# Kernel optimization log

Hardware: AMD Instinct MI355X
Metric: run time of the kernel (lower is better)

## Reference

```python
import jax, jax.numpy as jnp
import numpy as np

N_NODES = 50000
N_EDGES = 600000
D_IN = 128
D = 128
N_REL = 2
N_LAYERS = 3


def rgcn_conv(h, src, dst, edge_type, weight, root, bias):
    # PyG RGCNConv (no bases), aggr='mean' per relation:
    # out_i = h_i @ root + bias + sum_r mean_{j in N_r(i)} h_j @ W_r
    out = h @ root + bias                      # [N, D]
    hs = h[src]                                # [E, D] gather once
    for r in range(N_REL):
        mask = (edge_type == r).astype(h.dtype)          # [E]
        agg = jax.ops.segment_sum(hs * mask[:, None], dst, num_segments=N_NODES)  # [N, D]
        cnt = jax.ops.segment_sum(mask, dst, num_segments=N_NODES)                # [N]
        mean = agg / jnp.maximum(cnt, 1.0)[:, None]
        out = out + mean @ weight[r]
    return out


def setup_inputs() -> dict:
    key = jax.random.key(0)
    ks = jax.random.split(key, 10)
    x = jax.random.normal(ks[0], (N_NODES, D_IN), dtype=jnp.float32)
    edge_index = jax.random.randint(ks[1], (2, N_EDGES), 0, N_NODES, dtype=jnp.int64)
    edge_attr = jax.random.normal(ks[2], (N_EDGES, N_REL), dtype=jnp.float32)
    # input projection f: Linear(D_IN, D); stored as [D_IN, D] (apply as x @ Wf + bf)
    Wf = jax.random.normal(ks[3], (D_IN, D), dtype=jnp.float32) / np.sqrt(D_IN)
    bf = jnp.zeros((D,), dtype=jnp.float32)
    # per-layer RGCNConv params, stacked over layers
    conv_weight = jax.random.normal(ks[4], (N_LAYERS, N_REL, D, D), dtype=jnp.float32) / np.sqrt(D)
    conv_root = jax.random.normal(ks[5], (N_LAYERS, D, D), dtype=jnp.float32) / np.sqrt(D)
    conv_bias = jnp.zeros((N_LAYERS, D), dtype=jnp.float32)
    return {"x": x, "edge_index": edge_index, "edge_attr": edge_attr,
            "Wf": Wf, "bf": bf, "conv_weight": conv_weight,
            "conv_root": conv_root, "conv_bias": conv_bias}


def reference(x, edge_index, edge_attr, Wf, bf, conv_weight, conv_root, conv_bias):
    src, dst = edge_index[0], edge_index[1]
    edge_type = jnp.argmax(edge_attr, axis=1)           # [E]
    h = jax.nn.relu(x @ Wf + bf)                        # [N, D]
    for l in range(N_LAYERS):
        h = rgcn_conv(h, src, dst, edge_type, conv_weight[l], conv_root[l], conv_bias[l])
        h = jax.nn.relu(h)
    return h
```

## Files before the change

### kernel.cpp

```cpp
#include <hip/hip_runtime.h>
#include <hip/hip_bf16.h>

#define NN 50000
#define NE 600000
#define D 128
#define NREL 2
#define BM 128

typedef __attribute__((ext_vector_type(8))) short bf16x8;
typedef __attribute__((ext_vector_type(4))) float f32x4;

__device__ __forceinline__ float bf2f(short s) {
    return __uint_as_float(((unsigned int)(unsigned short)s) << 16);
}

__global__ void k_etype_count(const float* __restrict__ attr,
                              const int* __restrict__ dst,
                              int* __restrict__ etype,
                              int* __restrict__ cnt, int E) {
    int i = blockIdx.x * blockDim.x + threadIdx.x;
    if (i >= E) return;
    float2 a = reinterpret_cast<const float2*>(attr)[i];
    int r = (a.y > a.x) ? 1 : 0;
    etype[i] = r;
    atomicAdd(&cnt[r * NN + dst[i]], 1);
}

__global__ void k_inv(const int* __restrict__ cnt, float* __restrict__ inv) {
    int i = blockIdx.x * blockDim.x + threadIdx.x;
    if (i >= NREL * NN) return;
    int c = cnt[i];
    inv[i] = 1.0f / (float)(c > 1 ? c : 1);
}

__global__ void k_alloc(const int* __restrict__ cnt, int* __restrict__ off,
                        int* __restrict__ total) {
    int i = blockIdx.x * blockDim.x + threadIdx.x;
    if (i >= NREL * NN) return;
    off[i] = atomicAdd(total, cnt[i]);
}

__global__ void k_fill(const int* __restrict__ src, const int* __restrict__ dst,
                       const int* __restrict__ etype,
                       int* __restrict__ cursor, int* __restrict__ srcs, int E) {
    int i = blockIdx.x * blockDim.x + threadIdx.x;
    if (i >= E) return;
    int key = etype[i] * NN + dst[i];
    int pos = atomicAdd(&cursor[key], 1);
    srcs[pos] = src[i];
}

__global__ void k_cvt_x(const float* __restrict__ x,
                        __hip_bfloat16* __restrict__ xb, int n4) {
    int i = blockIdx.x * blockDim.x + threadIdx.x;
    if (i >= n4) return;
    float4 v = reinterpret_cast<const float4*>(x)[i];
    __hip_bfloat162 a = __float22bfloat162_rn(make_float2(v.x, v.y));
    __hip_bfloat162 b = __float22bfloat162_rn(make_float2(v.z, v.w));
    reinterpret_cast<__hip_bfloat162*>(xb)[i * 2 + 0] = a;
    reinterpret_cast<__hip_bfloat162*>(xb)[i * 2 + 1] = b;
}

__global__ void k_prep_w(const float* __restrict__ Wf,
                         const float* __restrict__ cw,
                         const float* __restrict__ cr,
                         __hip_bfloat16* __restrict__ wt) {
    int idx = blockIdx.x * blockDim.x + threadIdx.x;
    if (idx >= 16384 + 3 * 49152) return;
    float v;
    if (idx < 16384) {
        int n = idx >> 7, k = idx & 127;
        v = Wf[k * 128 + n];
    } else {
        int j = idx - 16384;
        int l = j / 49152; j %= 49152;
        int n = j / 384, k = j % 384;
        if (k < 128)      v = cr[((size_t)l * 128 + k) * 128 + n];
        else if (k < 256) v = cw[((size_t)(l * 2 + 0) * 128 + (k - 128)) * 128 + n];
        else              v = cw[((size_t)(l * 2 + 1) * 128 + (k - 256)) * 128 + n];
    }
    wt[idx] = __float2bfloat16(v);
}

__global__ __launch_bounds__(256)
void k_aggregate(const __hip_bfloat16* __restrict__ h,
                 const int* __restrict__ srcs,
                 const int* __restrict__ off, const int* __restrict__ cnt,
                 const float* __restrict__ inv,
                 __hip_bfloat16* __restrict__ agg) {
    int wid = (blockIdx.x * blockDim.x + threadIdx.x) >> 6;
    int lane = threadIdx.x & 63;
    if (wid >= NREL * NN) return;
    int start = off[wid], c = cnt[wid];
    int g = lane >> 4, l16 = lane & 15;

    int sv = (lane < c) ? srcs[start + lane] : 0;

    float acc[8];
#pragma unroll
    for (int i = 0; i < 8; i++) acc[i] = 0.f;

    for (int base = 0; base < c; base += 8) {
        int j0 = base + g, j1 = base + g + 4;
        int t0 = __shfl(sv, j0 & 63);
        int t1 = __shfl(sv, j1 & 63);
        int s0 = (j0 < 64) ? t0 : ((j0 < c) ? srcs[start + j0] : 0);
        int s1 = (j1 < 64) ? t1 : ((j1 < c) ? srcs[start + j1] : 0);
        if (j0 < c) {
            bf16x8 v0 = *reinterpret_cast<const bf16x8*>(
                h + (size_t)s0 * D + l16 * 8);
#pragma unroll
            for (int i = 0; i < 8; i++) acc[i] += bf2f(v0[i]);
        }
        if (j1 < c) {
            bf16x8 v1 = *reinterpret_cast<const bf16x8*>(
                h + (size_t)s1 * D + l16 * 8);
#pragma unroll
            for (int i = 0; i < 8; i++) acc[i] += bf2f(v1[i]);
        }
    }

#pragma unroll
    for (int i = 0; i < 8; i++) acc[i] += __shfl_xor(acc[i], 16);
#pragma unroll
    for (int i = 0; i < 8; i++) acc[i] += __shfl_xor(acc[i], 32);

    if (g == 0) {
        float sc = inv[wid];
        union { bf16x8 v; __hip_bfloat162 h2[4]; } o;
#pragma unroll
        for (int i = 0; i < 4; i++)
            o.h2[i] = __float22bfloat162_rn(
                make_float2(acc[2 * i] * sc, acc[2 * i + 1] * sc));
        *reinterpret_cast<bf16x8*>(agg + (size_t)wid * D + l16 * 8) = o.v;
    }
}

template <int KTOT, bool OUT_F32>
__global__ __launch_bounds__(256)
void k_gemm_mfma(const __hip_bfloat16* __restrict__ A0,
                 const __hip_bfloat16* __restrict__ A1,
                 const __hip_bfloat16* __restrict__ A2,
                 const __hip_bfloat16* __restrict__ Wt,
                 const float* __restrict__ bias,
                 void* __restrict__ outv, int N) {
    __shared__ uint4 sB4[1024];
    char* sB = (char*)sB4;
    const int tid = threadIdx.x;
    const int w = tid >> 6;
    const int l16 = tid & 15, lg = (tid & 63) >> 4;
    const __hip_bfloat16* As[3] = {A0, A1, A2};

    f32x4 acc[2][8];
#pragma unroll
    for (int m = 0; m < 2; m++)
#pragma unroll
        for (int n = 0; n < 8; n++) acc[m][n] = (f32x4)(0.f);

    const size_t row0 = (size_t)blockIdx.x * BM;
    const int NKB = KTOT / 64;
#pragma unroll
    for (int kb = 0; kb < NKB; ++kb) {
        const __hip_bfloat16* Ac = As[kb >> 1];
        const int koff = (kb & 1) * 64;
        bf16x8 afr[2][2];
#pragma unroll
        for (int mb = 0; mb < 2; ++mb)
#pragma unroll
            for (int kk = 0; kk < 2; ++kk) {
                int r = (int)row0 + w * 32 + mb * 16 + l16;
                if (r >= N) r = N - 1;
                afr[mb][kk] = *reinterpret_cast<const bf16x8*>(
                    Ac + (size_t)r * D + koff + kk * 32 + lg * 8);
            }
        __syncthreads();
        {
            int trow = tid >> 3;
            int tb = (tid & 7) * 16;
#pragma unroll
            for (int p = 0; p < 4; ++p) {
                int rr = trow + p * 32;
                uint4 v = *reinterpret_cast<const uint4*>(
                    (const char*)(Wt + (size_t)rr * KTOT + kb * 64) + tb);
                *reinterpret_cast<uint4*>(sB + rr * 128 + (tb ^ ((rr & 7) << 4))) = v;
            }
        }
        __syncthreads();
#pragma unroll
        for (int kk = 0; kk < 2; ++kk) {
#pragma unroll
            for (int nb = 0; nb < 8; ++nb) {
                int brow = nb * 16 + l16;
                int bcol = kk * 64 + lg * 16;
                bf16x8 bfr = *reinterpret_cast<const bf16x8*>(
                    sB + brow * 128 + (bcol ^ ((brow & 7) << 4)));
                acc[0][nb] = __builtin_amdgcn_mfma_f32_16x16x32_bf16(
                    afr[0][kk], bfr, acc[0][nb], 0, 0, 0);
                acc[1][nb] = __builtin_amdgcn_mfma_f32_16x16x32_bf16(
                    afr[1][kk], bfr, acc[1][nb], 0, 0, 0);
            }
        }
    }
#pragma unroll
    for (int nb = 0; nb < 8; ++nb) {
        int n = nb * 16 + l16;
        float bv = bias[n];
#pragma unroll
        for (int mb = 0; mb < 2; ++mb) {
#pragma unroll
            for (int r = 0; r < 4; ++r) {
                long grow = (long)row0 + w * 32 + mb * 16 + lg * 4 + r;
                if (grow < N) {
                    float v = acc[mb][nb][r] + bv;
                    v = v > 0.f ? v : 0.f;
                    if (OUT_F32)
                        ((float*)outv)[(size_t)grow * D + n] = v;
                    else
                        ((__hip_bfloat16*)outv)[(size_t)grow * D + n] =
                            __float2bfloat16(v);
                }
            }
        }
    }
}

extern "C" void kernel_launch(void* const* d_in, const int* in_sizes, int n_in,
                              void* d_out, int out_size, void* d_ws, size_t ws_size,
                              hipStream_t stream) {
    const float* x    = (const float*)d_in[0];
    const int*   ei   = (const int*)d_in[1];
    const float* attr = (const float*)d_in[2];
    const float* Wf   = (const float*)d_in[3];
    const float* bf   = (const float*)d_in[4];
    const float* cw   = (const float*)d_in[5];
    const float* cr   = (const float*)d_in[6];
    const float* cb   = (const float*)d_in[7];
    const int* src  = ei;
    const int* dstv = ei + NE;

    char* p = (char*)d_ws;
    __hip_bfloat16* h0   = (__hip_bfloat16*)p; p += (size_t)NN * D * 2;
    __hip_bfloat16* h1   = (__hip_bfloat16*)p; p += (size_t)NN * D * 2;
    __hip_bfloat16* aggb = (__hip_bfloat16*)p; p += (size_t)2 * NN * D * 2;
    __hip_bfloat16* xb   = (__hip_bfloat16*)p; p += (size_t)NN * D * 2;
    __hip_bfloat16* wt   = (__hip_bfloat16*)p; p += (size_t)(16384 + 3 * 49152) * 2;
    float* inv  = (float*)p;                p += (size_t)2 * NN * 4;
    int*   cnt  = (int*)p;                  p += (size_t)2 * NN * 4;
    int*   etyp = (int*)p;                  p += (size_t)NE * 4;
    int*   off  = (int*)p;                  p += (size_t)2 * NN * 4;
    int*   cur  = (int*)p;                  p += (size_t)2 * NN * 4;
    int*   srcs = (int*)p;                  p += (size_t)NE * 4;
    int*   total= (int*)p;

    float* outp = (float*)d_out;

    hipMemsetAsync(cnt, 0, (size_t)2 * NN * sizeof(int), stream);
    hipMemsetAsync(total, 0, sizeof(int), stream);
    k_etype_count<<<(NE + 255) / 256, 256, 0, stream>>>(attr, dstv, etyp, cnt, NE);
    k_inv<<<(2 * NN + 255) / 256, 256, 0, stream>>>(cnt, inv);
    k_alloc<<<(2 * NN + 255) / 256, 256, 0, stream>>>(cnt, off, total);
    hipMemcpyAsync(cur, off, (size_t)2 * NN * sizeof(int),
                   hipMemcpyDeviceToDevice, stream);
    k_fill<<<(NE + 255) / 256, 256, 0, stream>>>(src, dstv, etyp, cur, srcs, NE);
    k_cvt_x<<<(NN * D / 4 + 255) / 256, 256, 0, stream>>>(x, xb, NN * D / 4);
    k_prep_w<<<(16384 + 3 * 49152 + 255) / 256, 256, 0, stream>>>(Wf, cw, cr, wt);

    const int gblocks = (NN + BM - 1) / BM;
    k_gemm_mfma<128, false><<<gblocks, 256, 0, stream>>>(
        xb, xb, xb, wt, bf, h0, NN);

    const int ablocks = (2 * NN * 64 + 255) / 256;
    for (int l = 0; l < 3; ++l) {
        const __hip_bfloat16* hin = (l == 1) ? h1 : h0;
        k_aggregate<<<ablocks, 256, 0, stream>>>(hin, srcs, off, cnt, inv, aggb);
        const __hip_bfloat16* wl = wt + 16384 + (size_t)l * 49152;
        const float* bl = cb + (size_t)l * D;
        if (l == 2) {
            k_gemm_mfma<384, true><<<gblocks, 256, 0, stream>>>(
                hin, aggb, aggb + (size_t)NN * D, wl, bl, outp, NN);
        } else {
            __hip_bfloat16* hout = (l == 0) ? h1 : h0;
            k_gemm_mfma<384, false><<<gblocks, 256, 0, stream>>>(
                hin, aggb, aggb + (size_t)NN * D, wl, bl, hout, NN);
        }
    }
}
```

Before: 284.0 us.

## Fuse neighbor aggregation into per-layer GEMM via shared-memory staging

```diff
diff --git a/kernel.cpp b/kernel.cpp
--- a/kernel.cpp
+++ b/kernel.cpp
@@ -5,7 +5,6 @@
 #define NE 600000
 #define D 128
 #define NREL 2
-#define BM 128
 
 typedef __attribute__((ext_vector_type(8))) short bf16x8;
 typedef __attribute__((ext_vector_type(4))) float f32x4;
@@ -13,16 +12,21 @@
 __device__ __forceinline__ float bf2f(short s) {
     return __uint_as_float(((unsigned int)(unsigned short)s) << 16);
 }
-
-__global__ void k_etype_count(const float* __restrict__ attr,
-                              const int* __restrict__ dst,
-                              int* __restrict__ etype,
-                              int* __restrict__ cnt, int E) {
+__device__ __forceinline__ bf16x8 pack_bf8(const float* a) {
+    union { bf16x8 v; __hip_bfloat162 h2[4]; } o;
+#pragma unroll
+    for (int i = 0; i < 4; i++)
+        o.h2[i] = __float22bfloat162_rn(make_float2(a[2 * i], a[2 * i + 1]));
+    return o.v;
+}
+
+__global__ void k_count(const float* __restrict__ attr,
+                        const int* __restrict__ dst,
+                        int* __restrict__ cnt, int E) {
     int i = blockIdx.x * blockDim.x + threadIdx.x;
     if (i >= E) return;
     float2 a = reinterpret_cast<const float2*>(attr)[i];
     int r = (a.y > a.x) ? 1 : 0;
-    etype[i] = r;
     atomicAdd(&cnt[r * NN + dst[i]], 1);
 }
 
@@ -34,31 +38,23 @@
 }
 
 __global__ void k_alloc(const int* __restrict__ cnt, int* __restrict__ off,
-                        int* __restrict__ total) {
+                        int* __restrict__ cur, int* __restrict__ total) {
     int i = blockIdx.x * blockDim.x + threadIdx.x;
     if (i >= NREL * NN) return;
-    off[i] = atomicAdd(total, cnt[i]);
-}
-
-__global__ void k_fill(const int* __restrict__ src, const int* __restrict__ dst,
-                       const int* __restrict__ etype,
+    int o = atomicAdd(total, cnt[i]);
+    off[i] = o;
+    cur[i] = o;
+}
+
+__global__ void k_fill(const float* __restrict__ attr,
+                       const int* __restrict__ src, const int* __restrict__ dst,
                        int* __restrict__ cursor, int* __restrict__ srcs, int E) {
     int i = blockIdx.x * blockDim.x + threadIdx.x;
     if (i >= E) return;
-    int key = etype[i] * NN + dst[i];
-    int pos = atomicAdd(&cursor[key], 1);
+    float2 a = reinterpret_cast<const float2*>(attr)[i];
+    int r = (a.y > a.x) ? 1 : 0;
+    int pos = atomicAdd(&cursor[r * NN + dst[i]], 1);
     srcs[pos] = src[i];
-}
-
-__global__ void k_cvt_x(const float* __restrict__ x,
-                        __hip_bfloat16* __restrict__ xb, int n4) {
-    int i = blockIdx.x * blockDim.x + threadIdx.x;
-    if (i >= n4) return;
-    float4 v = reinterpret_cast<const float4*>(x)[i];
-    __hip_bfloat162 a = __float22bfloat162_rn(make_float2(v.x, v.y));
-    __hip_bfloat162 b = __float22bfloat162_rn(make_float2(v.z, v.w));
-    reinterpret_cast<__hip_bfloat162*>(xb)[i * 2 + 0] = a;
-    reinterpret_cast<__hip_bfloat162*>(xb)[i * 2 + 1] = b;
 }
 
 __global__ void k_prep_w(const float* __restrict__ Wf,
@@ -83,73 +79,15 @@
 }
 
 __global__ __launch_bounds__(256)
-void k_aggregate(const __hip_bfloat16* __restrict__ h,
-                 const int* __restrict__ srcs,
-                 const int* __restrict__ off, const int* __restrict__ cnt,
-                 const float* __restrict__ inv,
-                 __hip_bfloat16* __restrict__ agg) {
-    int wid = (blockIdx.x * blockDim.x + threadIdx.x) >> 6;
-    int lane = threadIdx.x & 63;
-    if (wid >= NREL * NN) return;
-    int start = off[wid], c = cnt[wid];
-    int g = lane >> 4, l16 = lane & 15;
-
-    int sv = (lane < c) ? srcs[start + lane] : 0;
-
-    float acc[8];
-#pragma unroll
-    for (int i = 0; i < 8; i++) acc[i] = 0.f;
-
-    for (int base = 0; base < c; base += 8) {
-        int j0 = base + g, j1 = base + g + 4;
-        int t0 = __shfl(sv, j0 & 63);
-        int t1 = __shfl(sv, j1 & 63);
-        int s0 = (j0 < 64) ? t0 : ((j0 < c) ? srcs[start + j0] : 0);
-        int s1 = (j1 < 64) ? t1 : ((j1 < c) ? srcs[start + j1] : 0);
-        if (j0 < c) {
-            bf16x8 v0 = *reinterpret_cast<const bf16x8*>(
-                h + (size_t)s0 * D + l16 * 8);
-#pragma unroll
-            for (int i = 0; i < 8; i++) acc[i] += bf2f(v0[i]);
-        }
-        if (j1 < c) {
-            bf16x8 v1 = *reinterpret_cast<const bf16x8*>(
-                h + (size_t)s1 * D + l16 * 8);
-#pragma unroll
-            for (int i = 0; i < 8; i++) acc[i] += bf2f(v1[i]);
-        }
-    }
-
-#pragma unroll
-    for (int i = 0; i < 8; i++) acc[i] += __shfl_xor(acc[i], 16);
-#pragma unroll
-    for (int i = 0; i < 8; i++) acc[i] += __shfl_xor(acc[i], 32);
-
-    if (g == 0) {
-        float sc = inv[wid];
-        union { bf16x8 v; __hip_bfloat162 h2[4]; } o;
-#pragma unroll
-        for (int i = 0; i < 4; i++)
-            o.h2[i] = __float22bfloat162_rn(
-                make_float2(acc[2 * i] * sc, acc[2 * i + 1] * sc));
-        *reinterpret_cast<bf16x8*>(agg + (size_t)wid * D + l16 * 8) = o.v;
-    }
-}
-
-template <int KTOT, bool OUT_F32>
-__global__ __launch_bounds__(256)
-void k_gemm_mfma(const __hip_bfloat16* __restrict__ A0,
-                 const __hip_bfloat16* __restrict__ A1,
-                 const __hip_bfloat16* __restrict__ A2,
+void k_gemm_proj(const float* __restrict__ X,
                  const __hip_bfloat16* __restrict__ Wt,
                  const float* __restrict__ bias,
-                 void* __restrict__ outv, int N) {
+                 __hip_bfloat16* __restrict__ out, int N) {
     __shared__ uint4 sB4[1024];
     char* sB = (char*)sB4;
     const int tid = threadIdx.x;
     const int w = tid >> 6;
     const int l16 = tid & 15, lg = (tid & 63) >> 4;
-    const __hip_bfloat16* As[3] = {A0, A1, A2};
 
     f32x4 acc[2][8];
 #pragma unroll
@@ -157,37 +95,36 @@
 #pragma unroll
         for (int n = 0; n < 8; n++) acc[m][n] = (f32x4)(0.f);
 
-    const size_t row0 = (size_t)blockIdx.x * BM;
-    const int NKB = KTOT / 64;
-#pragma unroll
-    for (int kb = 0; kb < NKB; ++kb) {
-        const __hip_bfloat16* Ac = As[kb >> 1];
-        const int koff = (kb & 1) * 64;
+    const int row0 = blockIdx.x * 128;
+#pragma unroll
+    for (int kb = 0; kb < 2; ++kb) {
         bf16x8 afr[2][2];
 #pragma unroll
         for (int mb = 0; mb < 2; ++mb)
 #pragma unroll
             for (int kk = 0; kk < 2; ++kk) {
-                int r = (int)row0 + w * 32 + mb * 16 + l16;
+                int r = row0 + w * 32 + mb * 16 + l16;
                 if (r >= N) r = N - 1;
-                afr[mb][kk] = *reinterpret_cast<const bf16x8*>(
-                    Ac + (size_t)r * D + koff + kk * 32 + lg * 8);
+                const float* p = X + (size_t)r * D + kb * 64 + kk * 32 + lg * 8;
+                float4 u0 = reinterpret_cast<const float4*>(p)[0];
+                float4 u1 = reinterpret_cast<const float4*>(p)[1];
+                float t[8] = {u0.x, u0.y, u0.z, u0.w, u1.x, u1.y, u1.z, u1.w};
+                afr[mb][kk] = pack_bf8(t);
             }
         __syncthreads();
         {
-            int trow = tid >> 3;
-            int tb = (tid & 7) * 16;
+            int trow = tid >> 3, tb = (tid & 7) * 16;
 #pragma unroll
             for (int p = 0; p < 4; ++p) {
                 int rr = trow + p * 32;
                 uint4 v = *reinterpret_cast<const uint4*>(
-                    (const char*)(Wt + (size_t)rr * KTOT + kb * 64) + tb);
+                    (const char*)(Wt + (size_t)rr * 128 + kb * 64) + tb);
                 *reinterpret_cast<uint4*>(sB + rr * 128 + (tb ^ ((rr & 7) << 4))) = v;
             }
         }
         __syncthreads();
 #pragma unroll
-        for (int kk = 0; kk < 2; ++kk) {
+        for (int kk = 0; kk < 2; ++kk)
 #pragma unroll
             for (int nb = 0; nb < 8; ++nb) {
                 int brow = nb * 16 + l16;
@@ -199,26 +136,158 @@
                 acc[1][nb] = __builtin_amdgcn_mfma_f32_16x16x32_bf16(
                     afr[1][kk], bfr, acc[1][nb], 0, 0, 0);
             }
-        }
     }
 #pragma unroll
     for (int nb = 0; nb < 8; ++nb) {
         int n = nb * 16 + l16;
         float bv = bias[n];
 #pragma unroll
-        for (int mb = 0; mb < 2; ++mb) {
+        for (int mb = 0; mb < 2; ++mb)
 #pragma unroll
             for (int r = 0; r < 4; ++r) {
-                long grow = (long)row0 + w * 32 + mb * 16 + lg * 4 + r;
+                int grow = row0 + w * 32 + mb * 16 + lg * 4 + r;
                 if (grow < N) {
                     float v = acc[mb][nb][r] + bv;
                     v = v > 0.f ? v : 0.f;
-                    if (OUT_F32)
-                        ((float*)outv)[(size_t)grow * D + n] = v;
-                    else
-                        ((__hip_bfloat16*)outv)[(size_t)grow * D + n] =
-                            __float2bfloat16(v);
+                    out[(size_t)grow * D + n] = __float2bfloat16(v);
                 }
+            }
+    }
+}
+
+template <bool OUT_F32>
+__global__ __launch_bounds__(256)
+void k_layer(const __hip_bfloat16* __restrict__ hin,
+             const int* __restrict__ srcs,
+             const int* __restrict__ off, const int* __restrict__ cnt,
+             const float* __restrict__ inv,
+             const __hip_bfloat16* __restrict__ Wt,
+             const float* __restrict__ bias,
+             void* __restrict__ outv) {
+    __shared__ char sAgg[128 * 256];
+    __shared__ uint4 sB4[1024];
+    char* sB = (char*)sB4;
+    const int tid = threadIdx.x;
+    const int row0 = blockIdx.x * 64;
+
+    {
+        const int grp = tid >> 3, l8 = tid & 7;
+        const char* hb = (const char*)hin;
+#pragma unroll
+        for (int bb = grp; bb < 128; bb += 32) {
+            const int rel = bb >> 6, lr = bb & 63;
+            const int row = row0 + lr;
+            float a[16];
+#pragma unroll
+            for (int i = 0; i < 16; i++) a[i] = 0.f;
+            float sc = 0.f;
+            if (row < NN) {
+                int wid = rel * NN + row;
+                int st = off[wid], c = cnt[wid];
+                sc = inv[wid];
+                int j = 0;
+                for (; j + 1 < c; j += 2) {
+                    int s0 = srcs[st + j], s1 = srcs[st + j + 1];
+                    const char* p0 = hb + (size_t)s0 * 256 + l8 * 32;
+                    const char* p1 = hb + (size_t)s1 * 256 + l8 * 32;
+                    bf16x8 v0 = *(const bf16x8*)p0;
+                    bf16x8 v1 = *(const bf16x8*)(p0 + 16);
+                    bf16x8 v2 = *(const bf16x8*)p1;
+                    bf16x8 v3 = *(const bf16x8*)(p1 + 16);
+#pragma unroll
+                    for (int i = 0; i < 8; i++) {
+                        a[i]     += bf2f(v0[i]) + bf2f(v2[i]);
+                        a[8 + i] += bf2f(v1[i]) + bf2f(v3[i]);
+                    }
+                }
+                if (j < c) {
+                    int s0 = srcs[st + j];
+                    const char* p0 = hb + (size_t)s0 * 256 + l8 * 32;
+                    bf16x8 v0 = *(const bf16x8*)p0;
+                    bf16x8 v1 = *(const bf16x8*)(p0 + 16);
+#pragma unroll
+                    for (int i = 0; i < 8; i++) {
+                        a[i]     += bf2f(v0[i]);
+                        a[8 + i] += bf2f(v1[i]);
+                    }
+                }
+            }
+            float t0[8], t1[8];
+#pragma unroll
+            for (int i = 0; i < 8; i++) { t0[i] = a[i] * sc; t1[i] = a[8 + i] * sc; }
+            const int swz = (bb & 7) << 4;
+            char* dstp = sAgg + bb * 256;
+            *reinterpret_cast<bf16x8*>(dstp + ((l8 * 32) ^ swz))      = pack_bf8(t0);
+            *reinterpret_cast<bf16x8*>(dstp + ((l8 * 32 + 16) ^ swz)) = pack_bf8(t1);
+        }
+    }
+
+    const int w = tid >> 6, l16 = tid & 15, lg = (tid & 63) >> 4;
+    f32x4 acc[8];
+#pragma unroll
+    for (int n = 0; n < 8; n++) acc[n] = (f32x4)(0.f);
+
+    const int r_loc = w * 16 + l16;
+#pragma unroll
+    for (int kb = 0; kb < 6; ++kb) {
+        bf16x8 afr[2];
+        if (kb < 2) {
+            int r = row0 + r_loc; if (r >= NN) r = NN - 1;
+#pragma unroll
+            for (int kk = 0; kk < 2; ++kk)
+                afr[kk] = *reinterpret_cast<const bf16x8*>(
+                    hin + (size_t)r * D + kb * 64 + kk * 32 + lg * 8);
+        } else {
+            int rel = (kb - 2) >> 1;
+            int koff = ((kb - 2) & 1) * 64;
+            int bb = rel * 64 + r_loc;
+            int swz = (bb & 7) << 4;
+#pragma unroll
+            for (int kk = 0; kk < 2; ++kk) {
+                int bc = (koff + kk * 32 + lg * 8) * 2;
+                afr[kk] = *reinterpret_cast<const bf16x8*>(
+                    sAgg + bb * 256 + (bc ^ swz));
+            }
+        }
+        __syncthreads();
+        {
+            int trow = tid >> 3, tb = (tid & 7) * 16;
+#pragma unroll
+            for (int p = 0; p < 4; ++p) {
+                int rr = trow + p * 32;
+                uint4 v = *reinterpret_cast<const uint4*>(
+                    (const char*)(Wt + (size_t)rr * 384 + kb * 64) + tb);
+                *reinterpret_cast<uint4*>(sB + rr * 128 + (tb ^ ((rr & 7) << 4))) = v;
+            }
+        }
+        __syncthreads();
+#pragma unroll
+        for (int kk = 0; kk < 2; ++kk)
+#pragma unroll
+            for (int nb = 0; nb < 8; ++nb) {
+                int brow = nb * 16 + l16;
+                int bcol = kk * 64 + lg * 16;
+                bf16x8 bfr = *reinterpret_cast<const bf16x8*>(
+                    sB + brow * 128 + (bcol ^ ((brow & 7) << 4)));
+                acc[nb] = __builtin_amdgcn_mfma_f32_16x16x32_bf16(
+                    afr[kk], bfr, acc[nb], 0, 0, 0);
+            }
+    }
+#pragma unroll
+    for (int nb = 0; nb < 8; ++nb) {
+        int n = nb * 16 + l16;
+        float bv = bias[n];
+#pragma unroll
+        for (int r = 0; r < 4; ++r) {
+            int grow = row0 + w * 16 + lg * 4 + r;
+            if (grow < NN) {
+                float v = acc[nb][r] + bv;
+                v = v > 0.f ? v : 0.f;
+                if (OUT_F32)
+                    ((float*)outv)[(size_t)grow * D + n] = v;
+                else
+                    ((__hip_bfloat16*)outv)[(size_t)grow * D + n] =
+                        __float2bfloat16(v);
             }
         }
     }
@@ -239,14 +308,11 @@
     const int* dstv = ei + NE;
 
     char* p = (char*)d_ws;
-    __hip_bfloat16* h0   = (__hip_bfloat16*)p; p += (size_t)NN * D * 2;
-    __hip_bfloat16* h1   = (__hip_bfloat16*)p; p += (size_t)NN * D * 2;
-    __hip_bfloat16* aggb = (__hip_bfloat16*)p; p += (size_t)2 * NN * D * 2;
-    __hip_bfloat16* xb   = (__hip_bfloat16*)p; p += (size_t)NN * D * 2;
-    __hip_bfloat16* wt   = (__hip_bfloat16*)p; p += (size_t)(16384 + 3 * 49152) * 2;
+    __hip_bfloat16* h0 = (__hip_bfloat16*)p; p += (size_t)NN * D * 2;
+    __hip_bfloat16* h1 = (__hip_bfloat16*)p; p += (size_t)NN * D * 2;
+    __hip_bfloat16* wt = (__hip_bfloat16*)p; p += (size_t)(16384 + 3 * 49152) * 2;
     float* inv  = (float*)p;                p += (size_t)2 * NN * 4;
     int*   cnt  = (int*)p;                  p += (size_t)2 * NN * 4;
-    int*   etyp = (int*)p;                  p += (size_t)NE * 4;
     int*   off  = (int*)p;                  p += (size_t)2 * NN * 4;
     int*   cur  = (int*)p;                  p += (size_t)2 * NN * 4;
     int*   srcs = (int*)p;                  p += (size_t)NE * 4;
@@ -256,32 +322,26 @@
 
     hipMemsetAsync(cnt, 0, (size_t)2 * NN * sizeof(int), stream);
     hipMemsetAsync(total, 0, sizeof(int), stream);
-    k_etype_count<<<(NE + 255) / 256, 256, 0, stream>>>(attr, dstv, etyp, cnt, NE);
+    k_count<<<(NE + 255) / 256, 256, 0, stream>>>(attr, dstv, cnt, NE);
     k_inv<<<(2 * NN + 255) / 256, 256, 0, stream>>>(cnt, inv);
-    k_alloc<<<(2 * NN + 255) / 256, 256, 0, stream>>>(cnt, off, total);
-    hipMemcpyAsync(cur, off, (size_t)2 * NN * sizeof(int),
-                   hipMemcpyDeviceToDevice, stream);
-    k_fill<<<(NE + 255) / 256, 256, 0, stream>>>(src, dstv, etyp, cur, srcs, NE);
-    k_cvt_x<<<(NN * D / 4 + 255) / 256, 256, 0, stream>>>(x, xb, NN * D / 4);
+    k_alloc<<<(2 * NN + 255) / 256, 256, 0, stream>>>(cnt, off, cur, total);
+    k_fill<<<(NE + 255) / 256, 256, 0, stream>>>(attr, src, dstv, cur, srcs, NE);
     k_prep_w<<<(16384 + 3 * 49152 + 255) / 256, 256, 0, stream>>>(Wf, cw, cr, wt);
 
-    const int gblocks = (NN + BM - 1) / BM;
-    k_gemm_mfma<128, false><<<gblocks, 256, 0, stream>>>(
-        xb, xb, xb, wt, bf, h0, NN);
-
-    const int ablocks = (2 * NN * 64 + 255) / 256;
+    k_gemm_proj<<<(NN + 127) / 128, 256, 0, stream>>>(x, wt, bf, h0, NN);
+
+    const int lblocks = (NN + 63) / 64;
     for (int l = 0; l < 3; ++l) {
         const __hip_bfloat16* hin = (l == 1) ? h1 : h0;
-        k_aggregate<<<ablocks, 256, 0, stream>>>(hin, srcs, off, cnt, inv, aggb);
         const __hip_bfloat16* wl = wt + 16384 + (size_t)l * 49152;
         const float* bl = cb + (size_t)l * D;
         if (l == 2) {
-            k_gemm_mfma<384, true><<<gblocks, 256, 0, stream>>>(
-                hin, aggb, aggb + (size_t)NN * D, wl, bl, outp, NN);
+            k_layer<true><<<lblocks, 256, 0, stream>>>(
+                hin, srcs, off, cnt, inv, wl, bl, outp);
         } else {
             __hip_bfloat16* hout = (l == 0) ? h1 : h0;
-            k_gemm_mfma<384, false><<<gblocks, 256, 0, stream>>>(
-                hin, aggb, aggb + (size_t)NN * D, wl, bl, hout, NN);
-        }
-    }
-}
+            k_layer<false><<<lblocks, 256, 0, stream>>>(
+                hin, srcs, off, cnt, inv, wl, bl, hout);
+        }
+    }
+}
```

New measurement: 289.4 us. No clear change (+1.9%).
